# Kernel tuning notes

Measured on AMD Instinct MI355X. Metric: run time of the kernel, lower is better.

## Reference

```python
import jax, jax.numpy as jnp
import numpy as np

TWN_THRESHOLD_FACTOR = 0.05
BN_EPS = 1e-5


def ternary_quantize(w):
    # threshold = 0.05 * max|w| (detached); q in {-1, 0, +1}
    t = TWN_THRESHOLD_FACTOR * jnp.max(jnp.abs(jax.lax.stop_gradient(w)))
    return (w > t).astype(w.dtype) - (w < -t).astype(w.dtype)


def conv2d(x, w, b):
    q = ternary_quantize(w)
    y = jax.lax.conv_general_dilated(x, q, (1, 1), 'VALID',
                                     dimension_numbers=('NCHW', 'OIHW', 'NCHW'))
    return y + b[None, :, None, None]


def linear(x, w, b):
    q = ternary_quantize(w)
    return x @ q.T + b


def bn_train(x, gamma, beta, axes):
    # training-mode batch norm (biased variance), matches torch BN in train()
    mean = jnp.mean(x, axis=axes, keepdims=True)
    var = jnp.var(x, axis=axes, keepdims=True)
    xhat = (x - mean) * jax.lax.rsqrt(var + BN_EPS)
    shape = [1] * x.ndim
    shape[1] = x.shape[1]
    return xhat * gamma.reshape(shape) + beta.reshape(shape)


def maxpool2(x):
    return jax.lax.reduce_window(x, -jnp.inf, jax.lax.max,
                                 (1, 1, 2, 2), (1, 1, 2, 2), 'VALID')


def setup_inputs() -> dict:
    key = jax.random.key(0)
    ks = jax.random.split(key, 8)
    B, Cin, H, W = 512, 1, 28, 28
    C1, C2, K = 64, 128, 5
    FLAT, F1, F2 = 4 * 4 * C2, 512, 10
    inp = {
        'x': jax.random.normal(ks[0], (B, Cin, H, W), jnp.float32),
        'conv1_w': jax.random.normal(ks[1], (C1, Cin, K, K), jnp.float32) * (1.0 / np.sqrt(Cin * K * K)),
        'conv1_b': jax.random.normal(ks[2], (C1,), jnp.float32) * 0.05,
        'bn1_g': jnp.ones((C1,), jnp.float32),
        'bn1_b': jnp.zeros((C1,), jnp.float32),
        'conv2_w': jax.random.normal(ks[3], (C2, C1, K, K), jnp.float32) * (1.0 / np.sqrt(C1 * K * K)),
        'conv2_b': jax.random.normal(ks[4], (C2,), jnp.float32) * 0.05,
        'bn2_g': jnp.ones((C2,), jnp.float32),
        'bn2_b': jnp.zeros((C2,), jnp.float32),
        'fc1_w': jax.random.normal(ks[5], (F1, FLAT), jnp.float32) * (1.0 / np.sqrt(FLAT)),
        'fc1_b': jax.random.normal(ks[6], (F1,), jnp.float32) * 0.05,
        'bn3_g': jnp.ones((F1,), jnp.float32),
        'bn3_b': jnp.zeros((F1,), jnp.float32),
        'fc2_w': jax.random.normal(ks[7], (F2, F1), jnp.float32) * (1.0 / np.sqrt(F1)),
        'fc2_b': jnp.zeros((F2,), jnp.float32),
    }
    return inp


def reference(x, conv1_w, conv1_b, bn1_g, bn1_b, conv2_w, conv2_b, bn2_g, bn2_b,
              fc1_w, fc1_b, bn3_g, bn3_b, fc2_w, fc2_b):
    h = jax.nn.relu(bn_train(conv2d(x, conv1_w, conv1_b), bn1_g, bn1_b, (0, 2, 3)))
    h = maxpool2(h)  # [B, 64, 12, 12]
    h = jax.nn.relu(bn_train(conv2d(h, conv2_w, conv2_b), bn2_g, bn2_b, (0, 2, 3)))
    h = maxpool2(h)  # [B, 128, 4, 4]
    h = h.reshape(h.shape[0], -1)  # [B, 2048]
    h = jax.nn.relu(bn_train(linear(h, fc1_w, fc1_b), bn3_g, bn3_b, (0,)))
    return linear(h, fc2_w, fc2_b)  # [B, 10]
```

## Files before the change

kernel.cpp:

```cpp
#include <hip/hip_runtime.h>
#include <stdint.h>

#define EPS 1e-5f

typedef short v8s __attribute__((ext_vector_type(8)));
typedef float v4f __attribute__((ext_vector_type(4)));

static const size_t W2F   = 8192;
static const size_t WF2F  = 212992;
static const size_t A_F   = 262144;
static const size_t PMN2F = 4980736;
static const size_t B_F   = 19136512;
static const size_t WF1T  = B_F + 1048576;

#define P_C1 1024
#define P_F2 1025
#define P_C2 1040
#define P_F1 1240

__device__ inline unsigned short f2bf(float f) {
    unsigned u = __float_as_uint(f);
    return (unsigned short)((u + 0x7FFF + ((u >> 16) & 1)) >> 16);
}

__device__ __forceinline__ void stage16(const unsigned short* g, unsigned short* l) {
    __builtin_amdgcn_global_load_lds(
        (const __attribute__((address_space(1))) unsigned int*)g,
        (__attribute__((address_space(3))) unsigned int*)l, 16, 0, 0);
}

__global__ void k_absz(const float* __restrict__ c1w, const float* __restrict__ c2w,
                       const float* __restrict__ f1w, const float* __restrict__ f2w,
                       float* __restrict__ wsf) {
    __shared__ float sm4[4];
    int blk = blockIdx.x;
    if (blk >= 384) {
        if (blk < 386) {
            int i = (blk - 384) * 256 + threadIdx.x + 16;
            if (i < 528) wsf[i] = 0.f;
        } else {
            int i = (blk - 386) * 256 + threadIdx.x + 1808;
            if (i < 2832) wsf[i] = 0.f;
        }
        return;
    }
    const float* w; int n; int nb; int bi; float* out;
    if (blk == 0)       { w = c1w; n = 1600;    nb = 1;   bi = 0;         out = wsf + P_C1; }
    else if (blk == 1)  { w = f2w; n = 5120;    nb = 1;   bi = 0;         out = wsf + P_F2; }
    else if (blk < 194) { w = c2w; n = 204800;  nb = 192; bi = blk - 2;   out = wsf + P_C2 + bi; }
    else                { w = f1w; n = 1048576; nb = 190; bi = blk - 194; out = wsf + P_F1 + bi; }
    float m = 0.f;
    for (int i = bi * 256 + threadIdx.x; i < n; i += nb * 256)
        m = fmaxf(m, fabsf(w[i]));
    #pragma unroll
    for (int o = 32; o; o >>= 1) m = fmaxf(m, __shfl_down(m, o));
    if ((threadIdx.x & 63) == 0) sm4[threadIdx.x >> 6] = m;
    __syncthreads();
    if (threadIdx.x == 0)
        *out = fmaxf(fmaxf(sm4[0], sm4[1]), fmaxf(sm4[2], sm4[3]));
}

__global__ __launch_bounds__(512) void k_mid(const float* __restrict__ x,
                                             const float* __restrict__ c1w,
                                             const float* __restrict__ c2w,
                                             const float* __restrict__ f1w,
                                             const float* __restrict__ f2w,
                                             float* __restrict__ wsf,
                                             unsigned* __restrict__ pmn1,
                                             unsigned short* __restrict__ w2u,
                                             unsigned short* __restrict__ wf1,
                                             float* __restrict__ wf2) {
    int blk = blockIdx.x;
    int tid = threadIdx.x;
    if (blk >= 512) {
        if (blk < 612) {
            float m = 0.f;
            for (int i = 0; i < 192; ++i) m = fmaxf(m, wsf[P_C2 + i]);
            float t = 0.05f * m;
            for (int i = (blk - 512) * 512 + tid; i < 204800; i += 100 * 512) {
                int j    = i & 7;
                int lane = (i >> 3) & 63;
                int mt   = (i >> 9) & 7;
                int ks   = (i >> 12) & 1;
                int p    = i >> 13;
                int c  = mt * 16 + (lane & 15);
                int ci = ks * 32 + (lane >> 4) * 8 + j;
                float v = c2w[c * 1600 + ci * 25 + p];
                w2u[i] = (v > t) ? (unsigned short)0x3F80
                                 : ((v < -t) ? (unsigned short)0xBF80 : (unsigned short)0);
            }
        } else if (blk < 868) {
            float m = 0.f;
            for (int i = 0; i < 190; ++i) m = fmaxf(m, wsf[P_F1 + i]);
            float t = 0.05f * m;
            for (int i = (blk - 612) * 512 + tid; i < 1048576; i += 256 * 512) {
                float v = f1w[i];
                unsigned short q = (v > t) ? (unsigned short)0x3F80
                                 : ((v < -t) ? (unsigned short)0xBF80 : (unsigned short)0);
                int f = i >> 11, k = i & 2047;
                int ft = f >> 4, fm = f & 15;
                int ks = k >> 5, kr = k & 31;
                int lane = (kr >> 3) * 16 + fm;
                wf1[((size_t)(ks * 32 + ft) * 64 + lane) * 8 + (kr & 7)] = q;
            }
        } else {
            float t = 0.05f * wsf[P_F2];
            for (int i = tid; i < 5120; i += 512) {
                float v = f2w[i];
                wf2[i] = (float)((v > t) - (v < -t));
            }
        }
        return;
    }
    __shared__ float xs[784];
    __shared__ float red[2][8][64];
    int b = blk;
    const float4* xim = (const float4*)(x + (size_t)b * 784);
    for (int i = tid; i < 196; i += 512) ((float4*)xs)[i] = xim[i];
    int c  = tid & 63;
    int wv = tid >> 6;
    float w[25];
    {
        float t = 0.05f * wsf[P_C1];
        const float* src = c1w + c * 25;
        #pragma unroll
        for (int k = 0; k < 25; ++k) {
            float v = src[k];
            w[k] = (float)((v > t) - (v < -t));
        }
    }
    __syncthreads();
    unsigned* ob = pmn1 + (size_t)b * 9216;
    float s = 0.f, s2 = 0.f;
    int ph = 0, pw = wv;
    for (int it = 0; it < 18; ++it) {
        const float* xp = xs + (ph * 2) * 28 + pw * 2;
        float win[36];
        #pragma unroll
        for (int i = 0; i < 6; ++i)
            #pragma unroll
            for (int j = 0; j < 3; ++j) {
                float2 t2 = *(const float2*)(xp + i * 28 + j * 2);
                win[i * 6 + j * 2] = t2.x; win[i * 6 + j * 2 + 1] = t2.y;
            }
        float v00 = 0.f, v01 = 0.f, v10 = 0.f, v11 = 0.f;
        #pragma unroll
        for (int i = 0; i < 5; ++i)
            #pragma unroll
            for (int j = 0; j < 5; ++j) {
                float wk = w[i * 5 + j];
                v00 = fmaf(win[i * 6 + j],           wk, v00);
                v01 = fmaf(win[i * 6 + j + 1],       wk, v01);
                v10 = fmaf(win[(i + 1) * 6 + j],     wk, v10);
                v11 = fmaf(win[(i + 1) * 6 + j + 1], wk, v11);
            }
        s  += v00 + v01 + v10 + v11;
        s2 += v00 * v00 + v01 * v01 + v10 * v10 + v11 * v11;
        float mx = fmaxf(fmaxf(v00, v01), fmaxf(v10, v11));
        float mn = fminf(fminf(v00, v01), fminf(v10, v11));
        ob[(ph * 12 + pw) * 64 + c] = ((unsigned)f2bf(mx) << 16) | (unsigned)f2bf(mn);
        pw += 8; if (pw >= 12) { pw -= 12; ++ph; }
    }
    red[0][wv][c] = s; red[1][wv][c] = s2;
    __syncthreads();
    if (tid < 64) {
        float S = 0.f, S2 = 0.f;
        #pragma unroll
        for (int i = 0; i < 8; ++i) { S += red[0][i][tid]; S2 += red[1][i][tid]; }
        atomicAdd(&wsf[16 + tid], S);
        atomicAdd(&wsf[80 + tid], S2);
    }
}

__global__ __launch_bounds__(256) void k_conv2(const unsigned* __restrict__ pmn1,
                                               const unsigned short* __restrict__ wfrag,
                                               const float* __restrict__ c1sum,
                                               const float* __restrict__ c1ssq,
                                               const float* __restrict__ g1,
                                               const float* __restrict__ b1,
                                               float* __restrict__ pmn,
                                               float* __restrict__ sum,
                                               float* __restrict__ ssq) {
    __shared__ unsigned short xs[144 * 76];
    __shared__ unsigned short wb[2][4096];
    __shared__ float reds[2][64], redq[2][64];
    int b     = blockIdx.x >> 1;
    int mhalf = blockIdx.x & 1;
    int tid  = threadIdx.x;
    int lane = tid & 63;
    int wave = tid >> 6;
    int nh = wave & 1, kp = wave >> 1;

    int ch0 = (tid & 15) * 4;
    float scv[4], shv[4];
    {
        const float invN = 1.f / 294912.f;
        #pragma unroll
        for (int j = 0; j < 4; ++j) {
            int ch = ch0 + j;
            float mean = c1sum[ch] * invN;
            float var  = c1ssq[ch] * invN - mean * mean;
            scv[j] = g1[ch] * rsqrtf(var + EPS);
            shv[j] = b1[ch] - mean * scv[j];
        }
    }
    const uint4* srcp = (const uint4*)(pmn1 + (size_t)b * 9216);
    for (int it = 0; it < 9; ++it) {
        int i = it * 256 + tid;
        int r = i >> 4;
        uint4 u4 = srcp[i];
        unsigned long long pack = 0;
        #pragma unroll
        for (int j = 0; j < 4; ++j) {
            unsigned u = (&u4.x)[j];
            float mx = __uint_as_float(u & 0xffff0000u);
            float mn = __uint_as_float(u << 16);
            float v = (scv[j] > 0.f) ? mx : mn;
            unsigned short o = f2bf(fmaxf(0.f, fmaf(v, scv[j], shv[j])));
            pack |= ((unsigned long long)o) << (16 * j);
        }
        *(unsigned long long*)(&xs[r * 76 + ch0]) = pack;
    }
    int ksm0 = wave * 2, ksm1 = wave * 2 + 1;
    int ks0 = ksm0 >> 2, mt0 = ksm0 & 3;
    int ks1 = ksm1 >> 2, mt1 = ksm1 & 3;
    const unsigned short* g0 = wfrag + (size_t)(ks0 * 8 + mhalf * 4 + mt0) * 512 + lane * 8;
    const unsigned short* g1p = wfrag + (size_t)(ks1 * 8 + mhalf * 4 + mt1) * 512 + lane * 8;
    const int l0 = ks0 * 2048 + mt0 * 512 + lane * 8;
    const int l1 = ks1 * 2048 + mt1 * 512 + lane * 8;
    stage16(g0,  &wb[0][l0]);
    stage16(g1p, &wb[0][l1]);
    g0 += 8192; g1p += 8192;
    __syncthreads();

    int n = lane & 15, quad = lane >> 4;
    int ow = n & 7;
    int ohb0 = nh * 4 + (n >> 3);
    int col0 = kp * 32 + quad * 8;
    const int lb = kp * 2048 + lane * 8;
    int a0 = ohb0 * 912 + ow * 76 + col0;
    int kw = 0;
    v4f acc[4][2];
    #pragma unroll
    for (int mm = 0; mm < 4; ++mm) { acc[mm][0] = (v4f){0,0,0,0}; acc[mm][1] = (v4f){0,0,0,0}; }

    auto step = [&](const unsigned short* wbR, unsigned short* wbW, bool st) {
        if (st) {
            stage16(g0,  wbW + l0);
            stage16(g1p, wbW + l1);
            g0 += 8192; g1p += 8192;
        }
        v8s bf0 = *(const v8s*)(xs + a0);
        v8s bf1 = *(const v8s*)(xs + a0 + 1824);
        #pragma unroll
        for (int mm = 0; mm < 4; ++mm) {
            v8s af = *(const v8s*)(wbR + lb + mm * 512);
            acc[mm][0] = __builtin_amdgcn_mfma_f32_16x16x32_bf16(af, bf0, acc[mm][0], 0, 0, 0);
            acc[mm][1] = __builtin_amdgcn_mfma_f32_16x16x32_bf16(af, bf1, acc[mm][1], 0, 0, 0);
        }
        __syncthreads();
        a0 += (kw == 4) ? 608 : 76;
        kw = (kw == 4) ? 0 : kw + 1;
    };
    #pragma unroll 1
    for (int pp = 0; pp < 12; ++pp) {
        step(&wb[0][0], &wb[1][0], true);
        step(&wb[1][0], &wb[0][0], true);
    }
    step(&wb[0][0], &wb[1][0], false);

    float* mbuf = (float*)xs;
    if (kp == 1) {
        float* d = mbuf + (nh * 64 + lane) * 36;
        #pragma unroll
        for (int mm = 0; mm < 4; ++mm) {
            *(v4f*)(d + mm * 8)     = acc[mm][0];
            *(v4f*)(d + mm * 8 + 4) = acc[mm][1];
        }
    }
    __syncthreads();
    if (kp == 0) {
        const float* s = mbuf + (nh * 64 + lane) * 36;
        #pragma unroll
        for (int mm = 0; mm < 4; ++mm) {
            acc[mm][0] += *(const v4f*)(s + mm * 8);
            acc[mm][1] += *(const v4f*)(s + mm * 8 + 4);
        }
        float* po = pmn + (size_t)b * 4096;
        #pragma unroll
        for (int mm = 0; mm < 4; ++mm) {
            int cl0 = mm * 16 + quad * 4;
            #pragma unroll
            for (int r = 0; r < 4; ++r) {
                int cl = cl0 + r;
                int cc = mhalf * 64 + cl;
                float sA = 0.f, s2A = 0.f;
                #pragma unroll
                for (int bf = 0; bf < 2; ++bf) {
                    float v = acc[mm][bf][r];
                    float pm = fmaxf(v, __shfl_xor(v, 1));
                    float pn = fminf(v, __shfl_xor(v, 1));
                    pm = fmaxf(pm, __shfl_xor(pm, 8));
                    pn = fminf(pn, __shfl_xor(pn, 8));
                    if (((n & 1) == 0) && (n < 8)) {
                        int psp = (nh * 2 + bf) * 4 + (n >> 1);
                        *(float2*)(&po[(cc * 16 + psp) * 2]) = make_float2(pm, pn);
                    }
                    float s = v, s2 = v * v;
                    #pragma unroll
                    for (int m = 1; m < 16; m <<= 1) { s += __shfl_xor(s, m); s2 += __shfl_xor(s2, m); }
                    sA += s; s2A += s2;
                }
                if (n == 0) { reds[nh][cl] = sA; redq[nh][cl] = s2A; }
            }
        }
    }
    __syncthreads();
    if (tid < 64) {
        atomicAdd(&sum[mhalf * 64 + tid], reds[0][tid] + reds[1][tid]);
        atomicAdd(&ssq[mhalf * 64 + tid], redq[0][tid] + redq[1][tid]);
    }
}

__global__ void k_bnpool2(const float* __restrict__ pmn2, const float* __restrict__ c2sum,
                          const float* __restrict__ c2ssq, const float* __restrict__ g2,
                          const float* __restrict__ b2, unsigned short* __restrict__ xfrag) {
    int i = blockIdx.x * 256 + threadIdx.x;
    int j    = i & 7;
    int lane = (i >> 3) & 63;
    int bt   = (i >> 9) & 31;
    int ks   = i >> 14;
    int b = bt * 16 + (lane & 15);
    int k = ks * 32 + (lane >> 4) * 8 + j;
    int c = k >> 4, psp = k & 15;
    float2 mm = *(const float2*)(&pmn2[((size_t)b * 2048 + c * 16 + psp) * 2]);
    float mean = c2sum[c] * (1.f / 32768.f);
    float var  = c2ssq[c] * (1.f / 32768.f) - mean * mean;
    float sc = g2[c] * rsqrtf(var + EPS);
    float sh = b2[c] - mean * sc;
    float v = (sc > 0.f) ? mm.x : mm.y;
    xfrag[i] = f2bf(fmaxf(0.f, fmaf(v, sc, sh)));
}

__global__ __launch_bounds__(256) void k_fc1(const unsigned short* __restrict__ xfrag,
                                             const unsigned short* __restrict__ wfrag,
                                             float* __restrict__ out,
                                             float* __restrict__ sum,
                                             float* __restrict__ ssq) {
    int lane = threadIdx.x & 63;
    int wave = threadIdx.x >> 6;
    int ft = (blockIdx.x & 7) * 4 + wave;
    int bT = blockIdx.x >> 3;
    v4f acc = (v4f){0.f, 0.f, 0.f, 0.f};
    for (int ks = 0; ks < 64; ++ks) {
        v8s bfrag = *(const v8s*)(xfrag + ((size_t)(ks * 32 + bT) * 64 + lane) * 8);
        v8s afrag = *(const v8s*)(wfrag + ((size_t)(ks * 32 + ft) * 64 + lane) * 8);
        acc = __builtin_amdgcn_mfma_f32_16x16x32_bf16(afrag, bfrag, acc, 0, 0, 0);
    }
    int bb = bT * 16 + (lane & 15);
    int quad = lane >> 4;
    int f0 = ft * 16 + quad * 4;
    *(float4*)(&out[(size_t)bb * 512 + f0]) =
        make_float4(acc[0], acc[1], acc[2], acc[3]);
    #pragma unroll
    for (int r = 0; r < 4; ++r) {
        float s = acc[r], s2 = s * s;
        #pragma unroll
        for (int m = 1; m < 16; m <<= 1) { s += __shfl_xor(s, m); s2 += __shfl_xor(s2, m); }
        if ((lane & 15) == 0) { atomicAdd(&sum[f0 + r], s); atomicAdd(&ssq[f0 + r], s2); }
    }
}

__global__ __launch_bounds__(256) void k_fc2(const float* __restrict__ x,
                                             const float* __restrict__ w,
                                             const float* __restrict__ bias,
                                             const float* __restrict__ fsum,
                                             const float* __restrict__ fssq,
                                             const float* __restrict__ g3,
                                             const float* __restrict__ b3,
                                             float* __restrict__ out) {
    int lane = threadIdx.x & 63;
    int b = blockIdx.x * 4 + (threadIdx.x >> 6);
    float xa[8], sm[8], sq[8], ga[8], ba[8];
    {
        const float4* p;
        p = (const float4*)(x + (size_t)b * 512 + lane * 8);
        *(float4*)xa = p[0]; *(float4*)(xa + 4) = p[1];
        p = (const float4*)(fsum + lane * 8);
        *(float4*)sm = p[0]; *(float4*)(sm + 4) = p[1];
        p = (const float4*)(fssq + lane * 8);
        *(float4*)sq = p[0]; *(float4*)(sq + 4) = p[1];
        p = (const float4*)(g3 + lane * 8);
        *(float4*)ga = p[0]; *(float4*)(ga + 4) = p[1];
        p = (const float4*)(b3 + lane * 8);
        *(float4*)ba = p[0]; *(float4*)(ba + 4) = p[1];
    }
    float h[8];
    #pragma unroll
    for (int e = 0; e < 8; ++e) {
        float mean = sm[e] * (1.f / 512.f);
        float var  = sq[e] * (1.f / 512.f) - mean * mean;
        float sc = ga[e] * rsqrtf(var + EPS);
        float sh = ba[e] - mean * sc;
        h[e] = fmaxf(0.f, fmaf(xa[e], sc, sh));
    }
    #pragma unroll
    for (int j = 0; j < 10; ++j) {
        const float4* wp = (const float4*)(w + j * 512 + lane * 8);
        float4 w0 = wp[0], w1 = wp[1];
        float p = h[0] * w0.x + h[1] * w0.y + h[2] * w0.z + h[3] * w0.w
                + h[4] * w1.x + h[5] * w1.y + h[6] * w1.z + h[7] * w1.w;
        #pragma unroll
        for (int o = 32; o; o >>= 1) p += __shfl_down(p, o);
        if (lane == 0) out[b * 10 + j] = p + bias[j];
    }
}

extern "C" void kernel_launch(void* const* d_in, const int* in_sizes, int n_in,
                              void* d_out, int out_size, void* d_ws, size_t ws_size,
                              hipStream_t stream) {
    const float* x       = (const float*)d_in[0];
    const float* conv1_w = (const float*)d_in[1];
    const float* bn1_g   = (const float*)d_in[3];
    const float* bn1_b   = (const float*)d_in[4];
    const float* conv2_w = (const float*)d_in[5];
    const float* bn2_g   = (const float*)d_in[7];
    const float* bn2_b   = (const float*)d_in[8];
    const float* fc1_w   = (const float*)d_in[9];
    const float* bn3_g   = (const float*)d_in[11];
    const float* bn3_b   = (const float*)d_in[12];
    const float* fc2_w   = (const float*)d_in[13];
    const float* fc2_b   = (const float*)d_in[14];

    float* wsf = (float*)d_ws;

    float* c1_sum = wsf + 16,   * c1_ssq = wsf + 80;
    float* c2_sum = wsf + 272,  * c2_ssq = wsf + 400;
    float* f_sum  = wsf + 1808, * f_ssq  = wsf + 2320;

    unsigned short* w2u = (unsigned short*)(wsf + W2F);
    float* wf2 = wsf + WF2F;
    unsigned short* wf1 = (unsigned short*)(wsf + WF1T);
    unsigned* PMN1 = (unsigned*)(wsf + A_F);
    float* PMN2 = wsf + PMN2F;
    float* A    = wsf + A_F;
    unsigned short* xfrag = (unsigned short*)(wsf + B_F);

    k_absz<<<390, 256, 0, stream>>>(conv1_w, conv2_w, fc1_w, fc2_w, wsf);

    k_mid<<<869, 512, 0, stream>>>(x, conv1_w, conv2_w, fc1_w, fc2_w, wsf,
                                   PMN1, w2u, wf1, wf2);

    k_conv2<<<1024, 256, 0, stream>>>(PMN1, w2u, c1_sum, c1_ssq, bn1_g, bn1_b,
                                      PMN2, c2_sum, c2_ssq);

    k_bnpool2<<<4096, 256, 0, stream>>>(PMN2, c2_sum, c2_ssq, bn2_g, bn2_b, xfrag);

    k_fc1<<<256, 256, 0, stream>>>(xfrag, wf1, A, f_sum, f_ssq);

    k_fc2<<<128, 256, 0, stream>>>(A, wf2, fc2_b, f_sum, f_ssq, bn3_g, bn3_b,
                                   (float*)d_out);
}
```

Measured before the change: 210.7 us.

## Triple-buffer conv2 weight staging with prefetch distance two and vmcnt waits

Replaces the double-buffered weight staging in the conv2 kernel with a three-slot ring that prefetches two kernel positions ahead. It uses raw s_barrier and s_waitcnt vmcnt(2) so global loads stay in flight across an iteration instead of draining at every __syncthreads. The goal is to hide global-to-LDS latency behind the MFMA work. The cost is an extra 8 KB of LDS, which may lower occupancy, and the loop is no longer explicitly unroll-limited, so address arithmetic is recomputed each step. Correctness depends on stage16 being an async LDS load tracked by vmcnt.

```diff
diff --git a/kernel.cpp b/kernel.cpp
--- a/kernel.cpp
+++ b/kernel.cpp
@@ -182,7 +182,7 @@
                                                float* __restrict__ sum,
                                                float* __restrict__ ssq) {
     __shared__ unsigned short xs[144 * 76];
-    __shared__ unsigned short wb[2][4096];
+    __shared__ unsigned short wb[3][4096];
     __shared__ float reds[2][64], redq[2][64];
     int b     = blockIdx.x >> 1;
     int mhalf = blockIdx.x & 1;
@@ -221,54 +221,56 @@
         }
         *(unsigned long long*)(&xs[r * 76 + ch0]) = pack;
     }
-    int ksm0 = wave * 2, ksm1 = wave * 2 + 1;
-    int ks0 = ksm0 >> 2, mt0 = ksm0 & 3;
-    int ks1 = ksm1 >> 2, mt1 = ksm1 & 3;
-    const unsigned short* g0 = wfrag + (size_t)(ks0 * 8 + mhalf * 4 + mt0) * 512 + lane * 8;
-    const unsigned short* g1p = wfrag + (size_t)(ks1 * 8 + mhalf * 4 + mt1) * 512 + lane * 8;
-    const int l0 = ks0 * 2048 + mt0 * 512 + lane * 8;
-    const int l1 = ks1 * 2048 + mt1 * 512 + lane * 8;
-    stage16(g0,  &wb[0][l0]);
-    stage16(g1p, &wb[0][l1]);
-    g0 += 8192; g1p += 8192;
+    #pragma unroll
+    for (int pp = 0; pp < 2; ++pp) {
+        #pragma unroll
+        for (int h = 0; h < 2; ++h) {
+            int ksm = wave * 2 + h;
+            int ks = ksm >> 2, mt = ksm & 3;
+            const unsigned short* g = wfrag +
+                (size_t)((pp * 2 + ks) * 8 + mhalf * 4 + mt) * 512 + lane * 8;
+            stage16(g, &wb[pp][ks * 2048 + mt * 512 + lane * 8]);
+        }
+    }
     __syncthreads();
 
     int n = lane & 15, quad = lane >> 4;
     int ow = n & 7;
     int ohb0 = nh * 4 + (n >> 3);
     int col0 = kp * 32 + quad * 8;
-    const int lb = kp * 2048 + lane * 8;
-    int a0 = ohb0 * 912 + ow * 76 + col0;
-    int kw = 0;
     v4f acc[4][2];
     #pragma unroll
     for (int mm = 0; mm < 4; ++mm) { acc[mm][0] = (v4f){0,0,0,0}; acc[mm][1] = (v4f){0,0,0,0}; }
-
-    auto step = [&](const unsigned short* wbR, unsigned short* wbW, bool st) {
-        if (st) {
-            stage16(g0,  wbW + l0);
-            stage16(g1p, wbW + l1);
-            g0 += 8192; g1p += 8192;
-        }
-        v8s bf0 = *(const v8s*)(xs + a0);
-        v8s bf1 = *(const v8s*)(xs + a0 + 1824);
+    for (int p = 0; p < 25; ++p) {
+        int cur = p % 3;
+        int kh = p / 5, kw = p - (p / 5) * 5;
+        int col = (ow + kw) * 76 + col0;
+        v8s bf0 = *(const v8s*)(&xs[(ohb0 + kh) * 912 + col]);
+        v8s bf1 = *(const v8s*)(&xs[(ohb0 + 2 + kh) * 912 + col]);
         #pragma unroll
         for (int mm = 0; mm < 4; ++mm) {
-            v8s af = *(const v8s*)(wbR + lb + mm * 512);
+            v8s af = *(const v8s*)(&wb[cur][kp * 2048 + mm * 512 + lane * 8]);
             acc[mm][0] = __builtin_amdgcn_mfma_f32_16x16x32_bf16(af, bf0, acc[mm][0], 0, 0, 0);
             acc[mm][1] = __builtin_amdgcn_mfma_f32_16x16x32_bf16(af, bf1, acc[mm][1], 0, 0, 0);
         }
-        __syncthreads();
-        a0 += (kw == 4) ? 608 : 76;
-        kw = (kw == 4) ? 0 : kw + 1;
-    };
-    #pragma unroll 1
-    for (int pp = 0; pp < 12; ++pp) {
-        step(&wb[0][0], &wb[1][0], true);
-        step(&wb[1][0], &wb[0][0], true);
-    }
-    step(&wb[0][0], &wb[1][0], false);
-
+        asm volatile("s_barrier" ::: "memory");
+        if (p <= 22) {
+            int pn = p + 2, nxt = pn % 3;
+            #pragma unroll
+            for (int h = 0; h < 2; ++h) {
+                int ksm = wave * 2 + h;
+                int ks = ksm >> 2, mt = ksm & 3;
+                const unsigned short* g = wfrag +
+                    (size_t)((pn * 2 + ks) * 8 + mhalf * 4 + mt) * 512 + lane * 8;
+                stage16(g, &wb[nxt][ks * 2048 + mt * 512 + lane * 8]);
+            }
+            asm volatile("s_waitcnt vmcnt(2)" ::: "memory");
+        } else if (p == 23) {
+            asm volatile("s_waitcnt vmcnt(0)" ::: "memory");
+        }
+        if (p <= 23)
+            asm volatile("s_barrier" ::: "memory");
+    }
     float* mbuf = (float*)xs;
     if (kp == 1) {
         float* d = mbuf + (nh * 64 + lane) * 36;
```

Result: no change. 208.5 us (-1.1%).
